# Kernel optimization log

Hardware: AMD Instinct MI355X
Metric: run time of the kernel (lower is better)

## Reference

```python
import jax, jax.numpy as jnp
import numpy as np

H, W, C = 56, 56, 384
WS, SHIFT, HEADS = 7, 3, 12
HEAD_DIM = C // HEADS
SCALE = HEAD_DIM ** (-0.5)
NWIN = (H // WS) * (W // WS)  # 64 windows per image
NTOK = WS * WS                # 49 tokens per window
EPS = 1e-5


def _gen_mask():
    # static shift-window attention mask, computed with numpy (jit-safe constant)
    img = np.zeros((H, W))
    sl = (slice(0, -WS), slice(-WS, -SHIFT), slice(-SHIFT, None))
    cnt = 0
    for hs in sl:
        for ws in sl:
            img[hs, ws] = cnt
            cnt += 1
    mw = img.reshape(H // WS, WS, W // WS, WS).transpose(0, 2, 1, 3).reshape(-1, NTOK)
    diff = mw[:, None, :] - mw[:, :, None]  # (NWIN, NTOK, NTOK)
    return jnp.asarray(np.where(diff != 0, -100.0, 0.0), dtype=jnp.float32)

ATTN_MASK = _gen_mask()


def _layernorm(x, g, b):
    mu = jnp.mean(x, axis=-1, keepdims=True)
    var = jnp.var(x, axis=-1, keepdims=True)
    return (x - mu) * jax.lax.rsqrt(var + EPS) * g + b


def setup_inputs() -> dict:
    key = jax.random.key(0)
    ks = jax.random.split(key, 6)
    s = 0.02
    return {
        "x": jax.random.normal(ks[0], (16, H * W, C), dtype=jnp.float32),
        "ln1_g": jnp.ones((C,), jnp.float32),
        "ln1_b": jnp.zeros((C,), jnp.float32),
        "qkv_w": jax.random.normal(ks[1], (C, 3 * C), jnp.float32) * s,
        "proj_w": jax.random.normal(ks[2], (C, C), jnp.float32) * s,
        "proj_b": jnp.zeros((C,), jnp.float32),
        "ln2_g": jnp.ones((C,), jnp.float32),
        "ln2_b": jnp.zeros((C,), jnp.float32),
        "fc1_w": jax.random.normal(ks[3], (C, 4 * C), jnp.float32) * s,
        "fc1_b": jnp.zeros((4 * C,), jnp.float32),
        "fc2_w": jax.random.normal(ks[4], (4 * C, C), jnp.float32) * s,
        "fc2_b": jnp.zeros((C,), jnp.float32),
    }


def reference(x, ln1_g, ln1_b, qkv_w, proj_w, proj_b, ln2_g, ln2_b, fc1_w, fc1_b, fc2_w, fc2_b):
    B, N, _ = x.shape
    h = x
    y = _layernorm(x, ln1_g, ln1_b).reshape(B, H, W, C)
    # cyclic shift (note: source never rolls back; we match it)
    y = jnp.roll(y, shift=(-SHIFT, -SHIFT), axis=(1, 2))
    # window partition -> (B*NWIN, NTOK, C)
    y = y.reshape(B, H // WS, WS, W // WS, WS, C).transpose(0, 1, 3, 2, 4, 5)
    y = y.reshape(B * NWIN, NTOK, C)
    # qkv (no bias), split heads
    qkv = (y @ qkv_w).reshape(B * NWIN, NTOK, 3, HEADS, HEAD_DIM)
    qkv = qkv.transpose(2, 0, 3, 1, 4)  # (3, BW, heads, NTOK, hd)
    q, k, v = qkv[0], qkv[1], qkv[2]
    attn = jnp.einsum('whnd,whmd->whnm', q, k) * SCALE  # (BW, heads, NTOK, NTOK)
    attn = attn.reshape(B, NWIN, HEADS, NTOK, NTOK) + ATTN_MASK[None, :, None]
    attn = jax.nn.softmax(attn.reshape(B * NWIN, HEADS, NTOK, NTOK), axis=-1)
    o = jnp.einsum('whnm,whmd->whnd', attn, v)
    o = o.transpose(0, 2, 1, 3).reshape(B * NWIN, NTOK, C)
    o = o @ proj_w + proj_b
    # window reverse -> (B, N, C)
    o = o.reshape(B, H // WS, W // WS, WS, WS, C).transpose(0, 1, 3, 2, 4, 5)
    o = o.reshape(B, N, C)
    x1 = h + o
    # MLP (GELU after both fc1 and fc2, as in source)
    m = _layernorm(x1, ln2_g, ln2_b)
    m = jax.nn.gelu(m @ fc1_w + fc1_b, approximate=False)
    m = jax.nn.gelu(m @ fc2_w + fc2_b, approximate=False)
    return x1 + m
```

## Files before the change

kernel.cpp:

```cpp
#include <hip/hip_runtime.h>
#include <hip/hip_bf16.h>
#include <cstdint>
#include <cstddef>

#define C_DIM   384
#define NIMG    3136
#define MROWS   50176
#define QK_SCALE 0.17677669529663687f

using bf16x8 = __attribute__((ext_vector_type(8))) short;
using f32x4  = __attribute__((ext_vector_type(4))) float;

__device__ __forceinline__ short f2bf(float f) {
  union { float f; uint32_t u; } v; v.f = f;
  uint32_t r = (v.u + 0x7fffu + ((v.u >> 16) & 1u)) >> 16;
  return (short)(uint16_t)r;
}

__device__ __forceinline__ float bf2f(short s) {
  union { uint32_t u; float f; } v; v.u = ((uint32_t)(uint16_t)s) << 16;
  return v.f;
}

__device__ __forceinline__ void async_copy16(const void* g, void* l) {
  __builtin_amdgcn_global_load_lds(
      (const __attribute__((address_space(1))) void*)g,
      (__attribute__((address_space(3))) void*)l, 16, 0, 0);
}

__device__ __forceinline__ float gelu_exact(float x) {
  return 0.5f * x * (1.0f + erff(x * 0.7071067811865475f));
}

__global__ __launch_bounds__(256) void transpose_cast(
    const float* __restrict__ w, short* __restrict__ wt, int K, int N) {
  int idx = blockIdx.x * 256 + threadIdx.x;
  if (idx >= K * N) return;
  int k = idx / N;
  int n = idx - k * N;
  wt[(size_t)n * K + k] = f2bf(w[idx]);
}

template <typename IN>
__global__ __launch_bounds__(256) void ln_kernel(
    const IN* __restrict__ x, const float* __restrict__ g,
    const float* __restrict__ b, short* __restrict__ y, int windowed) {
  int token = blockIdx.x * 4 + (threadIdx.x >> 6);
  int lane = threadIdx.x & 63;
  size_t src;
  if (windowed) {
    int bw = token / 49;
    int tt = token - bw * 49;
    int bb = bw >> 6, w = bw & 63;
    int hs = (w >> 3) * 7 + tt / 7 + 3; if (hs >= 56) hs -= 56;
    int ws = (w & 7) * 7 + (tt % 7) + 3; if (ws >= 56) ws -= 56;
    src = (size_t)(bb * NIMG + hs * 56 + ws) * C_DIM;
  } else {
    src = (size_t)token * C_DIM;
  }
  const IN* xr = x + src;
  float v[6];
  float s = 0.f;
#pragma unroll
  for (int i = 0; i < 6; ++i) {
    if constexpr (sizeof(IN) == 4) v[i] = (float)xr[lane + i * 64];
    else v[i] = bf2f((short)xr[lane + i * 64]);
    s += v[i];
  }
#pragma unroll
  for (int m = 1; m < 64; m <<= 1) s += __shfl_xor(s, m);
  float mu = s * (1.0f / 384.0f);
  float var = 0.f;
#pragma unroll
  for (int i = 0; i < 6; ++i) { float d = v[i] - mu; var += d * d; }
#pragma unroll
  for (int m = 1; m < 64; m <<= 1) var += __shfl_xor(var, m);
  float rstd = rsqrtf(var * (1.0f / 384.0f) + 1e-5f);
  short* yr = y + (size_t)token * C_DIM;
#pragma unroll
  for (int i = 0; i < 6; ++i) {
    int c = lane + i * 64;
    yr[c] = f2bf((v[i] - mu) * rstd * g[c] + b[c]);
  }
}

template <int EPI>
__global__ __launch_bounds__(256, 4) void gemm_kernel(
    const short* __restrict__ A, const short* __restrict__ Bt,
    void* __restrict__ Out, const float* __restrict__ bias,
    const void* __restrict__ resid, int M, int N, int K) {
  __shared__ __align__(16) short lds[128 * 64 * 2];
  const int t = threadIdx.x;
  const int wave = t >> 6, lane = t & 63;
  const int lrow = lane & 15, quad = lane >> 4;
  const int wm = wave & 1, wn = wave >> 1;
  const int m0 = blockIdx.x * 128, n0 = blockIdx.y * 128;
  short* ldsA = lds;
  short* ldsB = lds + 128 * 64;

  f32x4 acc[4][4] = {};

  const int srow = t >> 3;
  const int spos = t & 7;

  for (int k0 = 0; k0 < K; k0 += 64) {
    __syncthreads();
#pragma unroll
    for (int i = 0; i < 4; ++i) {
      int row = i * 32 + srow;
      int ca = spos ^ (row & 7);
      async_copy16(A + (size_t)(m0 + row) * K + k0 + ca * 8,
                   ldsA + (i * 32 + wave * 8) * 64);
      async_copy16(Bt + (size_t)(n0 + row) * K + k0 + ca * 8,
                   ldsB + (i * 32 + wave * 8) * 64);
    }
    __syncthreads();
#pragma unroll
    for (int ks = 0; ks < 2; ++ks) {
      const int cb = ks * 4;
      bf16x8 af[4], bfr[4];
#pragma unroll
      for (int i = 0; i < 4; ++i) {
        int ra = wm * 64 + i * 16 + lrow;
        af[i] = *(const bf16x8*)(ldsA + ra * 64 + (((cb + quad) ^ (ra & 7)) * 8));
        int rb = wn * 64 + i * 16 + lrow;
        bfr[i] = *(const bf16x8*)(ldsB + rb * 64 + (((cb + quad) ^ (rb & 7)) * 8));
      }
#pragma unroll
      for (int i = 0; i < 4; ++i)
#pragma unroll
        for (int j = 0; j < 4; ++j)
          acc[i][j] = __builtin_amdgcn_mfma_f32_16x16x32_bf16(af[i], bfr[j],
                                                              acc[i][j], 0, 0, 0);
    }
  }

#pragma unroll
  for (int i = 0; i < 4; ++i) {
#pragma unroll
    for (int r = 0; r < 4; ++r) {
      int row = m0 + wm * 64 + i * 16 + quad * 4 + r;
      if (EPI == 1) {
        int bw = row / 49;
        int tt = row - bw * 49;
        int bb = bw >> 6, w = bw & 63;
        int nimg = ((w >> 3) * 7 + tt / 7) * 56 + (w & 7) * 7 + (tt % 7);
        size_t obase = ((size_t)(bb * NIMG + nimg)) * C_DIM;
#pragma unroll
        for (int j = 0; j < 4; ++j) {
          int col = n0 + wn * 64 + j * 16 + lrow;
          size_t oi = obase + col;
          ((short*)Out)[oi] =
              f2bf(acc[i][j][r] + bias[col] + ((const float*)resid)[oi]);
        }
      } else {
#pragma unroll
        for (int j = 0; j < 4; ++j) {
          int col = n0 + wn * 64 + j * 16 + lrow;
          float v = acc[i][j][r];
          if (EPI == 0) {
            ((short*)Out)[(size_t)row * N + col] = f2bf(v);
          } else if (EPI == 2) {
            ((short*)Out)[(size_t)row * N + col] = f2bf(gelu_exact(v + bias[col]));
          } else {
            size_t oi = (size_t)row * C_DIM + col;
            ((float*)Out)[oi] =
                bf2f(((const short*)resid)[oi]) + gelu_exact(v + bias[col]);
          }
        }
      }
    }
  }
}

__global__ __launch_bounds__(256) void attn_kernel(
    const short* __restrict__ qkv, short* __restrict__ o) {
  __shared__ __align__(16) short plds[4][64 * 72];
  const int wavei = threadIdx.x >> 6;
  const int lane = threadIdx.x & 63;
  const int gw = blockIdx.x * 4 + wavei;
  const int bw = gw / 12;
  const int h = gw - bw * 12;
  const int w = bw & 63;
  const int lrow = lane & 15, quad = lane >> 4;
  const short* base = qkv + (size_t)bw * 49 * 1152 + h * 32;

  bf16x8 qf[4], kf[4];
#pragma unroll
  for (int i = 0; i < 4; ++i) {
    int tq = i * 16 + lrow;
    const short* p = base + (size_t)tq * 1152 + quad * 8;
    qf[i] = *(const bf16x8*)p;
    kf[i] = *(const bf16x8*)(p + 384);
  }
  f32x4 sa[4][4] = {};
#pragma unroll
  for (int i = 0; i < 4; ++i)
#pragma unroll
    for (int j = 0; j < 4; ++j)
      sa[i][j] = __builtin_amdgcn_mfma_f32_16x16x32_bf16(qf[i], kf[j], sa[i][j], 0, 0, 0);

  int tl = lane < 49 ? lane : 0;
  int rr = tl / 7, cc = tl - rr * 7;
  int hs = (w >> 3) * 7 + rr;
  int ws = (w & 7) * 7 + cc;
  int id = (hs < 49 ? 0 : (hs < 53 ? 3 : 6)) + (ws < 49 ? 0 : (ws < 53 ? 1 : 2));

  int idn[4], idm[4][4];
#pragma unroll
  for (int j = 0; j < 4; ++j) idn[j] = __shfl(id, j * 16 + lrow);
#pragma unroll
  for (int i = 0; i < 4; ++i)
#pragma unroll
    for (int r = 0; r < 4; ++r) idm[i][r] = __shfl(id, i * 16 + quad * 4 + r);

#pragma unroll
  for (int i = 0; i < 4; ++i)
#pragma unroll
    for (int j = 0; j < 4; ++j)
#pragma unroll
      for (int r = 0; r < 4; ++r) {
        float v = sa[i][j][r] * QK_SCALE + (idm[i][r] == idn[j] ? 0.f : -100.f);
        sa[i][j][r] = (j * 16 + lrow < 49) ? v : -1e30f;
      }

#pragma unroll
  for (int i = 0; i < 4; ++i)
#pragma unroll
    for (int r = 0; r < 4; ++r) {
      float mx = -1e30f;
#pragma unroll
      for (int j = 0; j < 4; ++j) mx = fmaxf(mx, sa[i][j][r]);
#pragma unroll
      for (int m = 1; m < 16; m <<= 1) mx = fmaxf(mx, __shfl_xor(mx, m));
      float sum = 0.f;
#pragma unroll
      for (int j = 0; j < 4; ++j) {
        float e = exp2f((sa[i][j][r] - mx) * 1.44269504f);
        sa[i][j][r] = e;
        sum += e;
      }
#pragma unroll
      for (int m = 1; m < 16; m <<= 1) sum += __shfl_xor(sum, m);
      float inv = 1.0f / sum;
#pragma unroll
      for (int j = 0; j < 4; ++j) sa[i][j][r] *= inv;
    }

  short* pw = plds[wavei];
#pragma unroll
  for (int i = 0; i < 4; ++i)
#pragma unroll
    for (int r = 0; r < 4; ++r)
#pragma unroll
      for (int j = 0; j < 4; ++j)
        pw[(i * 16 + quad * 4 + r) * 72 + j * 16 + lrow] = f2bf(sa[i][j][r]);

  f32x4 oa[4][2] = {};
#pragma unroll
  for (int kk = 0; kk < 2; ++kk) {
    bf16x8 vf[2];
#pragma unroll
    for (int j2 = 0; j2 < 2; ++j2) {
#pragma unroll
      for (int jj = 0; jj < 8; ++jj) {
        int n = kk * 32 + quad * 8 + jj;
        vf[j2][jj] = (n < 49)
            ? base[768 + (size_t)n * 1152 + j2 * 16 + lrow]
            : (short)0;
      }
    }
#pragma unroll
    for (int i = 0; i < 4; ++i) {
      bf16x8 pf = *(const bf16x8*)(pw + (i * 16 + lrow) * 72 + kk * 32 + quad * 8);
#pragma unroll
      for (int j2 = 0; j2 < 2; ++j2)
        oa[i][j2] = __builtin_amdgcn_mfma_f32_16x16x32_bf16(pf, vf[j2], oa[i][j2], 0, 0, 0);
    }
  }

#pragma unroll
  for (int i = 0; i < 4; ++i)
#pragma unroll
    for (int j2 = 0; j2 < 2; ++j2)
#pragma unroll
      for (int r = 0; r < 4; ++r) {
        int m = i * 16 + quad * 4 + r;
        if (m < 49)
          o[((size_t)bw * 49 + m) * 384 + h * 32 + j2 * 16 + lrow] = f2bf(oa[i][j2][r]);
      }
}

extern "C" void kernel_launch(void* const* d_in, const int* in_sizes, int n_in,
                              void* d_out, int out_size, void* d_ws, size_t ws_size,
                              hipStream_t stream) {
  const float* x      = (const float*)d_in[0];
  const float* ln1_g  = (const float*)d_in[1];
  const float* ln1_b  = (const float*)d_in[2];
  const float* qkv_w  = (const float*)d_in[3];
  const float* proj_w = (const float*)d_in[4];
  const float* proj_b = (const float*)d_in[5];
  const float* ln2_g  = (const float*)d_in[6];
  const float* ln2_b  = (const float*)d_in[7];
  const float* fc1_w  = (const float*)d_in[8];
  const float* fc1_b  = (const float*)d_in[9];
  const float* fc2_w  = (const float*)d_in[10];
  const float* fc2_b  = (const float*)d_in[11];
  float* out = (float*)d_out;

  char* ws = (char*)d_ws;
  auto alloc = [&](size_t bytes) {
    char* p = ws;
    ws += (bytes + 255) & ~(size_t)255;
    return p;
  };
  short* qkv_wT  = (short*)alloc((size_t)1152 * 384 * 2);
  short* proj_wT = (short*)alloc((size_t)384 * 384 * 2);
  short* fc1_wT  = (short*)alloc((size_t)1536 * 384 * 2);
  short* fc2_wT  = (short*)alloc((size_t)384 * 1536 * 2);
  short* bufA    = (short*)alloc((size_t)MROWS * 384 * 2);
  short* x1      = (short*)alloc((size_t)MROWS * 384 * 2);
  short* bufB    = (short*)alloc((size_t)MROWS * 1536 * 2);

  transpose_cast<<<(384 * 1152) / 256, 256, 0, stream>>>(qkv_w, qkv_wT, 384, 1152);
  transpose_cast<<<(384 * 384) / 256, 256, 0, stream>>>(proj_w, proj_wT, 384, 384);
  transpose_cast<<<(384 * 1536) / 256, 256, 0, stream>>>(fc1_w, fc1_wT, 384, 1536);
  transpose_cast<<<(1536 * 384) / 256, 256, 0, stream>>>(fc2_w, fc2_wT, 1536, 384);

  ln_kernel<float><<<MROWS / 4, 256, 0, stream>>>(x, ln1_g, ln1_b, bufA, 1);

  gemm_kernel<0><<<dim3(392, 9), 256, 0, stream>>>(bufA, qkv_wT, bufB, nullptr,
                                                   nullptr, MROWS, 1152, 384);

  attn_kernel<<<3072, 256, 0, stream>>>(bufB, bufA);

  gemm_kernel<1><<<dim3(392, 3), 256, 0, stream>>>(bufA, proj_wT, x1, proj_b,
                                                   x, MROWS, 384, 384);

  ln_kernel<short><<<MROWS / 4, 256, 0, stream>>>(x1, ln2_g, ln2_b, bufA, 0);

  gemm_kernel<2><<<dim3(392, 12), 256, 0, stream>>>(bufA, fc1_wT, bufB, fc1_b,
                                                    nullptr, MROWS, 1536, 384);

  gemm_kernel<3><<<dim3(392, 3), 256, 0, stream>>>(bufB, fc2_wT, out, fc2_b,
                                                   x1, MROWS, 384, 1536);
}
```

Before: 565.9 us.

## Double-buffer GEMM LDS tiles and swizzle workgroup order across XCDs

New measurement: 572.7 us. No clear change (+1.2%).

```diff
diff --git a/kernel.cpp b/kernel.cpp
--- a/kernel.cpp
+++ b/kernel.cpp
@@ -85,36 +85,58 @@
 }
 
 template <int EPI>
-__global__ __launch_bounds__(256, 4) void gemm_kernel(
+__global__ __launch_bounds__(256, 2) void gemm_kernel(
     const short* __restrict__ A, const short* __restrict__ Bt,
     void* __restrict__ Out, const float* __restrict__ bias,
-    const void* __restrict__ resid, int M, int N, int K) {
-  __shared__ __align__(16) short lds[128 * 64 * 2];
+    const void* __restrict__ resid, int M, int N, int K, int nby) {
+  __shared__ __align__(16) short lds[2][128 * 64 * 2];
   const int t = threadIdx.x;
   const int wave = t >> 6, lane = t & 63;
   const int lrow = lane & 15, quad = lane >> 4;
   const int wm = wave & 1, wn = wave >> 1;
-  const int m0 = blockIdx.x * 128, n0 = blockIdx.y * 128;
-  short* ldsA = lds;
-  short* ldsB = lds + 128 * 64;
+
+  const int wg = (int)blockIdx.x;
+  const int swz = (wg & 7) * ((int)gridDim.x >> 3) + (wg >> 3);
+  const int mb = swz / nby;
+  const int nb = swz - mb * nby;
+  const int m0 = mb * 128, n0 = nb * 128;
 
   f32x4 acc[4][4] = {};
 
   const int srow = t >> 3;
   const int spos = t & 7;
 
-  for (int k0 = 0; k0 < K; k0 += 64) {
-    __syncthreads();
+  const int nt = K >> 6;
+
+  auto stage = [&](int buf, int k0) {
+    short* la = &lds[buf][0];
+    short* lb = la + 128 * 64;
 #pragma unroll
     for (int i = 0; i < 4; ++i) {
       int row = i * 32 + srow;
       int ca = spos ^ (row & 7);
       async_copy16(A + (size_t)(m0 + row) * K + k0 + ca * 8,
-                   ldsA + (i * 32 + wave * 8) * 64);
+                   la + (i * 32 + wave * 8) * 64);
       async_copy16(Bt + (size_t)(n0 + row) * K + k0 + ca * 8,
-                   ldsB + (i * 32 + wave * 8) * 64);
-    }
-    __syncthreads();
+                   lb + (i * 32 + wave * 8) * 64);
+    }
+  };
+
+  stage(0, 0);
+
+  for (int kt = 0; kt < nt; ++kt) {
+    __builtin_amdgcn_sched_barrier(0);
+    if (kt + 1 < nt) {
+      stage((kt + 1) & 1, (kt + 1) * 64);
+      asm volatile("s_waitcnt vmcnt(8)" ::: "memory");
+    } else {
+      asm volatile("s_waitcnt vmcnt(0)" ::: "memory");
+    }
+    __builtin_amdgcn_s_barrier();
+    __builtin_amdgcn_sched_barrier(0);
+
+    short* ldsA = &lds[kt & 1][0];
+    short* ldsB = ldsA + 128 * 64;
 #pragma unroll
     for (int ks = 0; ks < 2; ++ks) {
       const int cb = ks * 4;
@@ -126,13 +148,17 @@
         int rb = wn * 64 + i * 16 + lrow;
         bfr[i] = *(const bf16x8*)(ldsB + rb * 64 + (((cb + quad) ^ (rb & 7)) * 8));
       }
+      __builtin_amdgcn_s_setprio(1);
 #pragma unroll
       for (int i = 0; i < 4; ++i)
 #pragma unroll
         for (int j = 0; j < 4; ++j)
           acc[i][j] = __builtin_amdgcn_mfma_f32_16x16x32_bf16(af[i], bfr[j],
                                                               acc[i][j], 0, 0, 0);
-    }
+      __builtin_amdgcn_s_setprio(0);
+    }
+    __builtin_amdgcn_sched_barrier(0);
+    __builtin_amdgcn_s_barrier();
   }
 
 #pragma unroll
@@ -329,19 +355,19 @@
 
   ln_kernel<float><<<MROWS / 4, 256, 0, stream>>>(x, ln1_g, ln1_b, bufA, 1);
 
-  gemm_kernel<0><<<dim3(392, 9), 256, 0, stream>>>(bufA, qkv_wT, bufB, nullptr,
-                                                   nullptr, MROWS, 1152, 384);
+  gemm_kernel<0><<<392 * 9, 256, 0, stream>>>(bufA, qkv_wT, bufB, nullptr,
+                                              nullptr, MROWS, 1152, 384, 9);
 
   attn_kernel<<<3072, 256, 0, stream>>>(bufB, bufA);
 
-  gemm_kernel<1><<<dim3(392, 3), 256, 0, stream>>>(bufA, proj_wT, x1, proj_b,
-                                                   x, MROWS, 384, 384);
+  gemm_kernel<1><<<392 * 3, 256, 0, stream>>>(bufA, proj_wT, x1, proj_b,
+                                              x, MROWS, 384, 384, 3);
 
   ln_kernel<short><<<MROWS / 4, 256, 0, stream>>>(x1, ln2_g, ln2_b, bufA, 0);
 
-  gemm_kernel<2><<<dim3(392, 12), 256, 0, stream>>>(bufA, fc1_wT, bufB, fc1_b,
-                                                    nullptr, MROWS, 1536, 384);
-
-  gemm_kernel<3><<<dim3(392, 3), 256, 0, stream>>>(bufB, fc2_wT, out, fc2_b,
-                                                   x1, MROWS, 384, 1536);
-}
+  gemm_kernel<2><<<392 * 12, 256, 0, stream>>>(bufA, fc1_wT, bufB, fc1_b,
+                                               nullptr, MROWS, 1536, 384, 12);
+
+  gemm_kernel<3><<<392 * 3, 256, 0, stream>>>(bufB, fc2_wT, out, fc2_b,
+                                              x1, MROWS, 384, 1536, 3);
+}
```
